# Kernel tuning notes

Hardware: AMD Instinct MI355X
Metric: run time of the kernel (lower is better)

The kernel has to match this reference:

```python
import jax, jax.numpy as jnp
import numpy as np

D_MODEL = 1024
N_HEADS = 16
D_K = D_MODEL // N_HEADS


def setup_inputs() -> dict:
    key = jax.random.key(0)
    ks = jax.random.split(key, 9)
    B, S = 2, 2048
    scale = 1.0 / np.sqrt(D_MODEL)
    inp = {
        "X": jax.random.normal(ks[0], (B, S, D_MODEL), dtype=jnp.float32),
        "Wq": jax.random.normal(ks[1], (D_MODEL, D_MODEL), dtype=jnp.float32) * scale,
        "bq": jnp.zeros((D_MODEL,), dtype=jnp.float32),
        "Wk": jax.random.normal(ks[2], (D_MODEL, D_MODEL), dtype=jnp.float32) * scale,
        "bk": jnp.zeros((D_MODEL,), dtype=jnp.float32),
        "Wv": jax.random.normal(ks[3], (D_MODEL, D_MODEL), dtype=jnp.float32) * scale,
        "bv": jnp.zeros((D_MODEL,), dtype=jnp.float32),
        "Wo": jax.random.normal(ks[4], (D_MODEL, D_MODEL), dtype=jnp.float32) * scale,
        "bo": jnp.zeros((D_MODEL,), dtype=jnp.float32),
    }
    return inp


def reference(X, Wq, bq, Wk, bk, Wv, bv, Wo, bo):
    B, S, _ = X.shape
    # QKV projections (torch Linear: x @ W.T + b; here W stored as [in, out])
    Q = X @ Wq + bq
    K = X @ Wk + bk
    V = X @ Wv + bv
    # [B, S, H, Dk] -> [B, H, S, Dk]
    def split_heads(t):
        return t.reshape(B, S, N_HEADS, D_K).transpose(0, 2, 1, 3)
    Q, K, V = split_heads(Q), split_heads(K), split_heads(V)
    scores = jnp.einsum('bhqd,bhkd->bhqk', Q, K) / jnp.sqrt(jnp.float32(D_K))
    attn = jax.nn.softmax(scores, axis=-1)
    out = jnp.einsum('bhqk,bhkd->bhqd', attn, V)  # [B, H, S, Dk]
    out = out.transpose(0, 2, 1, 3).reshape(B, S, D_MODEL)
    return out @ Wo + bo
```

## Files before the change

### kernel.cpp

```cpp
#include <hip/hip_runtime.h>
#include <hip/hip_bf16.h>


typedef __attribute__((ext_vector_type(8))) short short8;
typedef __attribute__((ext_vector_type(4))) float f32x4;
typedef unsigned short u16;
typedef unsigned int u32;

static __device__ __forceinline__ u16 f2bf(float f) {
    union { float f; u32 u; } c; c.f = f;
    u32 u = c.u;
    u32 r = u + 0x7fffu + ((u >> 16) & 1u);
    return (u16)(r >> 16);
}
static __device__ __forceinline__ float bf2f(u16 x) {
    union { u32 u; float f; } c; c.u = ((u32)x) << 16;
    return c.f;
}

#define GL1(p) ((const __attribute__((address_space(1))) void*)(p))
#define LD3(p) ((__attribute__((address_space(3))) void*)(p))
static __device__ __forceinline__ void gld16(const void* g, void* l) {
    __builtin_amdgcn_global_load_lds(GL1(g), LD3(l), 16, 0, 0);
}

#define Q_PRESCALE 0.18033688011112042f

__global__ __launch_bounds__(256) void convert_x(const float* __restrict__ X,
                                                 u16* __restrict__ Xb) {
    int i = (blockIdx.x * 256 + threadIdx.x) * 4;
    float4 v = *reinterpret_cast<const float4*>(X + i);
    ushort4 o;
    o.x = f2bf(v.x); o.y = f2bf(v.y); o.z = f2bf(v.z); o.w = f2bf(v.w);
    *reinterpret_cast<ushort4*>(Xb + i) = o;
}

__global__ __launch_bounds__(256) void transpose_w(
    const float* __restrict__ W0, const float* __restrict__ W1,
    const float* __restrict__ W2, const float* __restrict__ W3,
    u16* __restrict__ T0, u16* __restrict__ T1,
    u16* __restrict__ T2, u16* __restrict__ T3)
{
    const float* W; u16* T;
    switch (blockIdx.z) {
        case 0: W = W0; T = T0; break;
        case 1: W = W1; T = T1; break;
        case 2: W = W2; T = T2; break;
        default: W = W3; T = T3; break;
    }
    __shared__ float tile[64][65];
    int t = threadIdx.x;
    int k0 = blockIdx.y * 64, n0 = blockIdx.x * 64;
    int r = t / 16, c4 = (t % 16) * 4;
    #pragma unroll
    for (int p = 0; p < 4; p++) {
        int row = p * 16 + r;
        float4 v = *reinterpret_cast<const float4*>(W + (k0 + row) * 1024 + n0 + c4);
        tile[row][c4 + 0] = v.x; tile[row][c4 + 1] = v.y;
        tile[row][c4 + 2] = v.z; tile[row][c4 + 3] = v.w;
    }
    __syncthreads();
    #pragma unroll
    for (int p = 0; p < 4; p++) {
        int nrow = p * 16 + r;
        ushort4 o;
        o.x = f2bf(tile[c4 + 0][nrow]); o.y = f2bf(tile[c4 + 1][nrow]);
        o.z = f2bf(tile[c4 + 2][nrow]); o.w = f2bf(tile[c4 + 3][nrow]);
        *reinterpret_cast<ushort4*>(T + (n0 + nrow) * 1024 + k0 + c4) = o;
    }
}

__global__ __launch_bounds__(256) void gemm_qkv(
    const u16* __restrict__ Xb,
    const u16* __restrict__ Wtq, const u16* __restrict__ Wtk, const u16* __restrict__ Wtv,
    const float* __restrict__ bq, const float* __restrict__ bk, const float* __restrict__ bv,
    u16* __restrict__ Qb, u16* __restrict__ Kb, u16* __restrict__ Vb)
{
    const u16* Wt; const float* bias; u16* dst; float osc;
    if (blockIdx.z == 0)      { Wt = Wtq; bias = bq; dst = Qb; osc = Q_PRESCALE; }
    else if (blockIdx.z == 1) { Wt = Wtk; bias = bk; dst = Kb; osc = 1.0f; }
    else                      { Wt = Wtv; bias = bv; dst = Vb; osc = 1.0f; }

    __shared__ __align__(16) u16 As[128 * 32];
    __shared__ __align__(16) u16 Bs[128 * 32];
    int t = threadIdx.x;
    int w = t >> 6, lane = t & 63, l15 = lane & 15, quad = lane >> 4;
    int wm = (w >> 1) * 64, wn = (w & 1) * 64;
    int row0 = blockIdx.y * 128, col0 = blockIdx.x * 128;

    int drow = lane >> 2;
    int gc8 = ((lane & 3) ^ (drow & 3) ^ ((drow >> 2) & 3)) * 8;

    int asw = ((quad ^ (l15 & 3) ^ ((l15 >> 2) & 3)) & 3) * 8;

    f32x4 acc[4][4];
    #pragma unroll
    for (int i = 0; i < 4; i++)
        #pragma unroll
        for (int j = 0; j < 4; j++)
            acc[i][j] = (f32x4){0.f, 0.f, 0.f, 0.f};

    for (int k0 = 0; k0 < 1024; k0 += 32) {
        __syncthreads();
        #pragma unroll
        for (int q = 0; q < 2; q++) {
            int rr = w * 32 + q * 16;
            gld16(&Xb[(row0 + rr + drow) * 1024 + k0 + gc8], &As[rr * 32]);
            gld16(&Wt[(col0 + rr + drow) * 1024 + k0 + gc8], &Bs[rr * 32]);
        }
        __syncthreads();
        short8 a[4], b[4];
        #pragma unroll
        for (int i = 0; i < 4; i++)
            a[i] = *reinterpret_cast<const short8*>(&As[(wm + i * 16 + l15) * 32 + asw]);
        #pragma unroll
        for (int j = 0; j < 4; j++)
            b[j] = *reinterpret_cast<const short8*>(&Bs[(wn + j * 16 + l15) * 32 + asw]);
        #pragma unroll
        for (int i = 0; i < 4; i++)
            #pragma unroll
            for (int j = 0; j < 4; j++)
                acc[i][j] = __builtin_amdgcn_mfma_f32_16x16x32_bf16(a[i], b[j], acc[i][j], 0, 0, 0);
    }
    #pragma unroll
    for (int i = 0; i < 4; i++) {
        int rowb = row0 + wm + i * 16 + quad * 4;
        #pragma unroll
        for (int j = 0; j < 4; j++) {
            int col = col0 + wn + j * 16 + l15;
            float bb = bias[col];
            int h = col >> 6, d = col & 63;
            #pragma unroll
            for (int r = 0; r < 4; r++) {
                int gr = rowb + r;
                int b_ = gr >> 11, s = gr & 2047;
                dst[(((b_ << 4) + h) * 2048 + s) * 64 + d] = f2bf((acc[i][j][r] + bb) * osc);
            }
        }
    }
}

__global__ __launch_bounds__(256) void transpose_v(const u16* __restrict__ Vb,
                                                   u16* __restrict__ Vtg) {
    int bh = blockIdx.y;
    int s0 = blockIdx.x * 64;
    __shared__ u16 tile[64][72];
    int t = threadIdx.x;
    const u16* src = Vb + bh * (2048 * 64);
    u16* dst = Vtg + bh * (64 * 2048);
    int sl = t >> 3, d8 = (t & 7) * 8;
    #pragma unroll
    for (int p = 0; p < 2; p++) {
        int row = p * 32 + sl;
        *reinterpret_cast<uint4*>(&tile[row][d8]) =
            *reinterpret_cast<const uint4*>(&src[(s0 + row) * 64 + d8]);
    }
    __syncthreads();
    #pragma unroll
    for (int p = 0; p < 2; p++) {
        int dr = p * 32 + sl;
        union { u16 s[8]; uint4 v; } pk;
        #pragma unroll
        for (int i = 0; i < 8; i++) pk.s[i] = tile[d8 + i][dr];
        *reinterpret_cast<uint4*>(&dst[dr * 2048 + s0 + d8]) = pk.v;
    }
}

__global__ __launch_bounds__(256) void attn(
    const u16* __restrict__ Qb, const u16* __restrict__ Kb,
    const u16* __restrict__ Vtg, u16* __restrict__ Opart, float* __restrict__ Lsum)
{
    int qt = blockIdx.x, bh = blockIdx.y, sp = blockIdx.z;
    int b_ = bh >> 4, h = bh & 15;
    const u16* Qp = Qb + bh * (2048 * 64);
    const u16* Kp = Kb + bh * (2048 * 64);
    const u16* Vp = Vtg + bh * (64 * 2048);
    u16* Op = Opart + sp * (4096 * 1024);
    float* Lp = Lsum + sp * (32 * 2048) + bh * 2048;

    __shared__ __align__(16) u16 Ks[64 * 64];
    __shared__ __align__(16) u16 Vt[64 * 64];
    __shared__ __align__(16) u16 Ps[128 * 64];

    int t = threadIdx.x, w = t >> 6, lane = t & 63, l15 = lane & 15, quad = lane >> 4;

    short8 qf[2][2];
    #pragma unroll
    for (int f = 0; f < 2; f++)
        #pragma unroll
        for (int ds = 0; ds < 2; ds++)
            qf[f][ds] = *reinterpret_cast<const short8*>(
                &Qp[(qt * 128 + w * 32 + f * 16 + l15) * 64 + ds * 32 + quad * 8]);

    int di = lane >> 3;
    int dc8 = ((lane & 7) ^ di) * 8;

    int rl = l15 & 7, rh = l15 >> 3;
    int koff[4][2];
    #pragma unroll
    for (int j = 0; j < 4; j++)
        #pragma unroll
        for (int ds = 0; ds < 2; ds++)
            koff[j][ds] = (j * 2 + rh) * 512 + rl * 64 + (((ds * 4 + quad) ^ rl) & 7) * 8;

    int pwt[2][4];
    #pragma unroll
    for (int f = 0; f < 2; f++)
        #pragma unroll
        for (int j = 0; j < 4; j++)
            pwt[f][j] = (w * 32 + f * 16 + l15) * 64 +
                        (((2 * j + (quad >> 1)) ^ rl) * 8) + (quad & 1) * 4;
    int prt[2][2];
    #pragma unroll
    for (int f = 0; f < 2; f++)
        #pragma unroll
        for (int ks = 0; ks < 2; ks++)
            prt[f][ks] = (w * 32 + f * 16 + l15) * 64 + (((4 * ks + quad) ^ rl) * 8);

    f32x4 acc[2][4];
    float lsum[2] = {0.f, 0.f};
    #pragma unroll
    for (int f = 0; f < 2; f++)
        #pragma unroll
        for (int j = 0; j < 4; j++) acc[f][j] = (f32x4){0.f, 0.f, 0.f, 0.f};

    for (int kt = 0; kt < 16; kt++) {
        int kbase = sp * 1024 + kt * 64;
        __syncthreads();
        #pragma unroll
        for (int sg = 0; sg < 2; sg++) {
            int seg = w * 2 + sg;
            gld16(&Kp[(kbase + seg * 8 + di) * 64 + dc8], &Ks[seg * 512]);
            gld16(&Vp[(seg * 8 + di) * 2048 + kbase + dc8], &Vt[seg * 512]);
        }
        __syncthreads();

        f32x4 sc[2][4];
        #pragma unroll
        for (int j = 0; j < 4; j++) {
            f32x4 s0 = (f32x4){0.f, 0.f, 0.f, 0.f};
            f32x4 s1 = (f32x4){0.f, 0.f, 0.f, 0.f};
            #pragma unroll
            for (int ds = 0; ds < 2; ds++) {
                short8 kf = *reinterpret_cast<const short8*>(&Ks[koff[j][ds]]);
                s0 = __builtin_amdgcn_mfma_f32_16x16x32_bf16(kf, qf[0][ds], s0, 0, 0, 0);
                s1 = __builtin_amdgcn_mfma_f32_16x16x32_bf16(kf, qf[1][ds], s1, 0, 0, 0);
            }
            sc[0][j] = s0; sc[1][j] = s1;
        }

        #pragma unroll
        for (int f = 0; f < 2; f++)
            #pragma unroll
            for (int j = 0; j < 4; j++) {
                float p0 = __builtin_amdgcn_exp2f(sc[f][j][0]);
                float p1 = __builtin_amdgcn_exp2f(sc[f][j][1]);
                float p2 = __builtin_amdgcn_exp2f(sc[f][j][2]);
                float p3 = __builtin_amdgcn_exp2f(sc[f][j][3]);
                lsum[f] += (p0 + p1) + (p2 + p3);
                union { float fv; u32 uv; } c0, c1, c2, c3;
                c0.fv = p0; c1.fv = p1; c2.fv = p2; c3.fv = p3;
                uint2 pk;
                pk.x = ((c0.uv + 0x8000u) >> 16) | ((c1.uv + 0x8000u) & 0xffff0000u);
                pk.y = ((c2.uv + 0x8000u) >> 16) | ((c3.uv + 0x8000u) & 0xffff0000u);
                *reinterpret_cast<uint2*>(&Ps[pwt[f][j]]) = pk;
            }

        #pragma unroll
        for (int ks = 0; ks < 2; ks++) {
            short8 pf0 = *reinterpret_cast<const short8*>(&Ps[prt[0][ks]]);
            short8 pf1 = *reinterpret_cast<const short8*>(&Ps[prt[1][ks]]);
            #pragma unroll
            for (int j = 0; j < 4; j++) {
                short8 vf = *reinterpret_cast<const short8*>(&Vt[koff[j][ks]]);
                acc[0][j] = __builtin_amdgcn_mfma_f32_16x16x32_bf16(pf0, vf, acc[0][j], 0, 0, 0);
                acc[1][j] = __builtin_amdgcn_mfma_f32_16x16x32_bf16(pf1, vf, acc[1][j], 0, 0, 0);
            }
        }
    }

    #pragma unroll
    for (int f = 0; f < 2; f++) {
        float s = lsum[f];
        s += __shfl_xor(s, 16);
        s += __shfl_xor(s, 32);
        lsum[f] = s;
    }
    if (quad == 0) {
        #pragma unroll
        for (int f = 0; f < 2; f++)
            Lp[qt * 128 + w * 32 + f * 16 + l15] = lsum[f];
    }

    #pragma unroll
    for (int f = 0; f < 2; f++)
        #pragma unroll
        for (int j = 0; j < 4; j++)
            #pragma unroll
            for (int r = 0; r < 4; r++) {
                int srow = qt * 128 + w * 32 + f * 16 + quad * 4 + r;
                Op[(b_ * 2048 + srow) * 1024 + h * 64 + j * 16 + l15] = f2bf(acc[f][j][r]);
            }
}

__global__ __launch_bounds__(256) void combine(
    const u16* __restrict__ O0, const u16* __restrict__ O1,
    const float* __restrict__ L0, const float* __restrict__ L1,
    u16* __restrict__ Ob)
{
    int idx8 = (blockIdx.x * 256 + threadIdx.x) * 8;
    int row = idx8 >> 10, col = idx8 & 1023;
    int b_ = row >> 11, s = row & 2047, h = col >> 6;
    int li = (b_ * 16 + h) * 2048 + s;
    float inv = 1.0f / (L0[li] + L1[li]);
    union { uint4 v; u16 s[8]; } ua, ub, uo;
    ua.v = *reinterpret_cast<const uint4*>(&O0[idx8]);
    ub.v = *reinterpret_cast<const uint4*>(&O1[idx8]);
    #pragma unroll
    for (int i = 0; i < 8; i++)
        uo.s[i] = f2bf((bf2f(ua.s[i]) + bf2f(ub.s[i])) * inv);
    *reinterpret_cast<uint4*>(&Ob[idx8]) = uo.v;
}

__global__ __launch_bounds__(256) void gemm_out(
    const u16* __restrict__ Ob, const u16* __restrict__ Wto,
    const float* __restrict__ bo, float* __restrict__ out)
{
    __shared__ __align__(16) u16 As[128 * 32];
    __shared__ __align__(16) u16 Bs[128 * 32];
    int t = threadIdx.x;
    int w = t >> 6, lane = t & 63, l15 = lane & 15, quad = lane >> 4;
    int wm = (w >> 1) * 64, wn = (w & 1) * 64;
    int row0 = blockIdx.y * 128, col0 = blockIdx.x * 128;

    int drow = lane >> 2;
    int gc8 = ((lane & 3) ^ (drow & 3) ^ ((drow >> 2) & 3)) * 8;
    int asw = ((quad ^ (l15 & 3) ^ ((l15 >> 2) & 3)) & 3) * 8;

    f32x4 acc[4][4];
    #pragma unroll
    for (int i = 0; i < 4; i++)
        #pragma unroll
        for (int j = 0; j < 4; j++)
            acc[i][j] = (f32x4){0.f, 0.f, 0.f, 0.f};

    for (int k0 = 0; k0 < 1024; k0 += 32) {
        __syncthreads();
        #pragma unroll
        for (int q = 0; q < 2; q++) {
            int rr = w * 32 + q * 16;
            gld16(&Ob[(row0 + rr + drow) * 1024 + k0 + gc8], &As[rr * 32]);
            gld16(&Wto[(col0 + rr + drow) * 1024 + k0 + gc8], &Bs[rr * 32]);
        }
        __syncthreads();
        short8 a[4], b[4];
        #pragma unroll
        for (int i = 0; i < 4; i++)
            a[i] = *reinterpret_cast<const short8*>(&As[(wm + i * 16 + l15) * 32 + asw]);
        #pragma unroll
        for (int j = 0; j < 4; j++)
            b[j] = *reinterpret_cast<const short8*>(&Bs[(wn + j * 16 + l15) * 32 + asw]);
        #pragma unroll
        for (int i = 0; i < 4; i++)
            #pragma unroll
            for (int j = 0; j < 4; j++)
                acc[i][j] = __builtin_amdgcn_mfma_f32_16x16x32_bf16(a[i], b[j], acc[i][j], 0, 0, 0);
    }
    #pragma unroll
    for (int i = 0; i < 4; i++) {
        int rowb = row0 + wm + i * 16 + quad * 4;
        #pragma unroll
        for (int j = 0; j < 4; j++) {
            int col = col0 + wn + j * 16 + l15;
            float bb = bo[col];
            #pragma unroll
            for (int r = 0; r < 4; r++)
                out[(rowb + r) * 1024 + col] = acc[i][j][r] + bb;
        }
    }
}

extern "C" void kernel_launch(void* const* d_in, const int* in_sizes, int n_in,
                              void* d_out, int out_size, void* d_ws, size_t ws_size,
                              hipStream_t stream) {
    const float* X  = (const float*)d_in[0];
    const float* Wq = (const float*)d_in[1];
    const float* bq = (const float*)d_in[2];
    const float* Wk = (const float*)d_in[3];
    const float* bk = (const float*)d_in[4];
    const float* Wv = (const float*)d_in[5];
    const float* bv = (const float*)d_in[6];
    const float* Wo = (const float*)d_in[7];
    const float* bo = (const float*)d_in[8];
    float* out = (float*)d_out;

    char* ws = (char*)d_ws;
    u16* Xb   = (u16*)(ws);
    u16* Wtq  = (u16*)(ws + (8u  << 20));
    u16* Wtk  = (u16*)(ws + (10u << 20));
    u16* Wtv  = (u16*)(ws + (12u << 20));
    u16* Wto  = (u16*)(ws + (14u << 20));
    u16* Qb   = (u16*)(ws + (16u << 20));
    u16* Kb   = (u16*)(ws + (24u << 20));
    u16* Vb   = (u16*)(ws + (32u << 20));
    u16* Vtg  = (u16*)(ws + (40u << 20));
    u16* Op   = (u16*)(ws + (48u << 20));
    float* Ls = (float*)(ws + (64u << 20));
    u16* Ob   = (u16*)(ws + (65u << 20));

    convert_x  <<<4096, 256, 0, stream>>>(X, Xb);
    transpose_w<<<dim3(16, 16, 4), 256, 0, stream>>>(Wq, Wk, Wv, Wo, Wtq, Wtk, Wtv, Wto);
    gemm_qkv   <<<dim3(8, 32, 3), 256, 0, stream>>>(Xb, Wtq, Wtk, Wtv, bq, bk, bv, Qb, Kb, Vb);
    transpose_v<<<dim3(32, 32), 256, 0, stream>>>(Vb, Vtg);
    attn       <<<dim3(16, 32, 2), 256, 0, stream>>>(Qb, Kb, Vtg, Op, Ls);
    combine    <<<2048, 256, 0, stream>>>(Op, Op + (4096 * 1024), Ls, Ls + (32 * 2048), Ob);
    gemm_out   <<<dim3(8, 32), 256, 0, stream>>>(Ob, Wto, bo, out);
}
```

Measured before the change: 225.8 us.

## Fuse prep kernels and write V transposed directly from QKV GEMM epilogue

Merges the X conversion and weight transpose into one prep launch, and has the QKV GEMM write V already transposed ([bh][d][s]) so the separate transpose_v kernel goes away. Q and K are now stored in natural [B*S, 1024] row-major layout, and the attention kernel indexes heads through a 1024 stride. The point is to cut two kernel launches and one full pass over V. It also switches the P-to-bf16 packing from round-to-nearest to truncation, which is cheaper but slightly less accurate.

Result: slower. 234.2 us (+3.7%).

```diff
diff --git a/kernel.cpp b/kernel.cpp
--- a/kernel.cpp
+++ b/kernel.cpp
@@ -26,31 +26,33 @@
 
 #define Q_PRESCALE 0.18033688011112042f
 
-__global__ __launch_bounds__(256) void convert_x(const float* __restrict__ X,
-                                                 u16* __restrict__ Xb) {
-    int i = (blockIdx.x * 256 + threadIdx.x) * 4;
-    float4 v = *reinterpret_cast<const float4*>(X + i);
-    ushort4 o;
-    o.x = f2bf(v.x); o.y = f2bf(v.y); o.z = f2bf(v.z); o.w = f2bf(v.w);
-    *reinterpret_cast<ushort4*>(Xb + i) = o;
-}
-
-__global__ __launch_bounds__(256) void transpose_w(
+__global__ __launch_bounds__(256) void prep(
+    const float* __restrict__ X, u16* __restrict__ Xb,
     const float* __restrict__ W0, const float* __restrict__ W1,
     const float* __restrict__ W2, const float* __restrict__ W3,
     u16* __restrict__ T0, u16* __restrict__ T1,
     u16* __restrict__ T2, u16* __restrict__ T3)
 {
+    int id = blockIdx.x;
+    int t = threadIdx.x;
+    if (id >= 1024) {
+        int i = (id - 1024) * 1024 + t * 4;
+        float4 v = *reinterpret_cast<const float4*>(X + i);
+        ushort4 o;
+        o.x = f2bf(v.x); o.y = f2bf(v.y); o.z = f2bf(v.z); o.w = f2bf(v.w);
+        *reinterpret_cast<ushort4*>(Xb + i) = o;
+        return;
+    }
     const float* W; u16* T;
-    switch (blockIdx.z) {
+    switch (id >> 8) {
         case 0: W = W0; T = T0; break;
         case 1: W = W1; T = T1; break;
         case 2: W = W2; T = T2; break;
         default: W = W3; T = T3; break;
     }
+    int rem = id & 255;
+    int n0 = (rem & 15) * 64, k0 = (rem >> 4) * 64;
     __shared__ float tile[64][65];
-    int t = threadIdx.x;
-    int k0 = blockIdx.y * 64, n0 = blockIdx.x * 64;
     int r = t / 16, c4 = (t % 16) * 4;
     #pragma unroll
     for (int p = 0; p < 4; p++) {
@@ -74,12 +76,12 @@
     const u16* __restrict__ Xb,
     const u16* __restrict__ Wtq, const u16* __restrict__ Wtk, const u16* __restrict__ Wtv,
     const float* __restrict__ bq, const float* __restrict__ bk, const float* __restrict__ bv,
-    u16* __restrict__ Qb, u16* __restrict__ Kb, u16* __restrict__ Vb)
+    u16* __restrict__ Qn, u16* __restrict__ Kn, u16* __restrict__ Vtg)
 {
-    const u16* Wt; const float* bias; u16* dst; float osc;
-    if (blockIdx.z == 0)      { Wt = Wtq; bias = bq; dst = Qb; osc = Q_PRESCALE; }
-    else if (blockIdx.z == 1) { Wt = Wtk; bias = bk; dst = Kb; osc = 1.0f; }
-    else                      { Wt = Wtv; bias = bv; dst = Vb; osc = 1.0f; }
+    const u16* Wt; const float* bias;
+    if (blockIdx.z == 0)      { Wt = Wtq; bias = bq; }
+    else if (blockIdx.z == 1) { Wt = Wtk; bias = bk; }
+    else                      { Wt = Wtv; bias = bv; }
 
     __shared__ __align__(16) u16 As[128 * 32];
     __shared__ __align__(16) u16 Bs[128 * 32];
@@ -90,7 +92,6 @@
 
     int drow = lane >> 2;
     int gc8 = ((lane & 3) ^ (drow & 3) ^ ((drow >> 2) & 3)) * 8;
-
     int asw = ((quad ^ (l15 & 3) ^ ((l15 >> 2) & 3)) & 3) * 8;
 
     f32x4 acc[4][4];
@@ -122,58 +123,49 @@
             for (int j = 0; j < 4; j++)
                 acc[i][j] = __builtin_amdgcn_mfma_f32_16x16x32_bf16(a[i], b[j], acc[i][j], 0, 0, 0);
     }
-    #pragma unroll
-    for (int i = 0; i < 4; i++) {
-        int rowb = row0 + wm + i * 16 + quad * 4;
-        #pragma unroll
-        for (int j = 0; j < 4; j++) {
-            int col = col0 + wn + j * 16 + l15;
-            float bb = bias[col];
-            int h = col >> 6, d = col & 63;
-            #pragma unroll
-            for (int r = 0; r < 4; r++) {
-                int gr = rowb + r;
-                int b_ = gr >> 11, s = gr & 2047;
-                dst[(((b_ << 4) + h) * 2048 + s) * 64 + d] = f2bf((acc[i][j][r] + bb) * osc);
-            }
-        }
-    }
-}
-
-__global__ __launch_bounds__(256) void transpose_v(const u16* __restrict__ Vb,
-                                                   u16* __restrict__ Vtg) {
-    int bh = blockIdx.y;
-    int s0 = blockIdx.x * 64;
-    __shared__ u16 tile[64][72];
-    int t = threadIdx.x;
-    const u16* src = Vb + bh * (2048 * 64);
-    u16* dst = Vtg + bh * (64 * 2048);
-    int sl = t >> 3, d8 = (t & 7) * 8;
-    #pragma unroll
-    for (int p = 0; p < 2; p++) {
-        int row = p * 32 + sl;
-        *reinterpret_cast<uint4*>(&tile[row][d8]) =
-            *reinterpret_cast<const uint4*>(&src[(s0 + row) * 64 + d8]);
-    }
-    __syncthreads();
-    #pragma unroll
-    for (int p = 0; p < 2; p++) {
-        int dr = p * 32 + sl;
-        union { u16 s[8]; uint4 v; } pk;
-        #pragma unroll
-        for (int i = 0; i < 8; i++) pk.s[i] = tile[d8 + i][dr];
-        *reinterpret_cast<uint4*>(&dst[dr * 2048 + s0 + d8]) = pk.v;
+
+    if (blockIdx.z == 2) {
+        #pragma unroll
+        for (int i = 0; i < 4; i++) {
+            int gr = row0 + wm + i * 16 + quad * 4;
+            int b_ = gr >> 11, s = gr & 2047;
+            #pragma unroll
+            for (int j = 0; j < 4; j++) {
+                int col = col0 + wn + j * 16 + l15;
+                int h = col >> 6, d = col & 63;
+                float bb = bias[col];
+                ushort4 pk;
+                pk.x = f2bf(acc[i][j][0] + bb);
+                pk.y = f2bf(acc[i][j][1] + bb);
+                pk.z = f2bf(acc[i][j][2] + bb);
+                pk.w = f2bf(acc[i][j][3] + bb);
+                *reinterpret_cast<ushort4*>(&Vtg[((b_ * 16 + h) * 64 + d) * 2048 + s]) = pk;
+            }
+        }
+    } else {
+        u16* dst = (blockIdx.z == 0) ? Qn : Kn;
+        float osc = (blockIdx.z == 0) ? Q_PRESCALE : 1.0f;
+        #pragma unroll
+        for (int i = 0; i < 4; i++) {
+            int rowb = row0 + wm + i * 16 + quad * 4;
+            #pragma unroll
+            for (int j = 0; j < 4; j++) {
+                int col = col0 + wn + j * 16 + l15;
+                float bb = bias[col];
+                #pragma unroll
+                for (int r = 0; r < 4; r++)
+                    dst[(rowb + r) * 1024 + col] = f2bf((acc[i][j][r] + bb) * osc);
+            }
+        }
     }
 }
 
 __global__ __launch_bounds__(256) void attn(
-    const u16* __restrict__ Qb, const u16* __restrict__ Kb,
+    const u16* __restrict__ Qn, const u16* __restrict__ Kn,
     const u16* __restrict__ Vtg, u16* __restrict__ Opart, float* __restrict__ Lsum)
 {
     int qt = blockIdx.x, bh = blockIdx.y, sp = blockIdx.z;
     int b_ = bh >> 4, h = bh & 15;
-    const u16* Qp = Qb + bh * (2048 * 64);
-    const u16* Kp = Kb + bh * (2048 * 64);
     const u16* Vp = Vtg + bh * (64 * 2048);
     u16* Op = Opart + sp * (4096 * 1024);
     float* Lp = Lsum + sp * (32 * 2048) + bh * 2048;
@@ -190,7 +182,8 @@
         #pragma unroll
         for (int ds = 0; ds < 2; ds++)
             qf[f][ds] = *reinterpret_cast<const short8*>(
-                &Qp[(qt * 128 + w * 32 + f * 16 + l15) * 64 + ds * 32 + quad * 8]);
+                &Qn[(b_ * 2048 + qt * 128 + w * 32 + f * 16 + l15) * 1024 +
+                    h * 64 + ds * 32 + quad * 8]);
 
     int di = lane >> 3;
     int dc8 = ((lane & 7) ^ di) * 8;
@@ -230,7 +223,8 @@
         #pragma unroll
         for (int sg = 0; sg < 2; sg++) {
             int seg = w * 2 + sg;
-            gld16(&Kp[(kbase + seg * 8 + di) * 64 + dc8], &Ks[seg * 512]);
+            gld16(&Kn[(b_ * 2048 + kbase + seg * 8 + di) * 1024 + h * 64 + dc8],
+                  &Ks[seg * 512]);
             gld16(&Vp[(seg * 8 + di) * 2048 + kbase + dc8], &Vt[seg * 512]);
         }
         __syncthreads();
@@ -261,8 +255,8 @@
                 union { float fv; u32 uv; } c0, c1, c2, c3;
                 c0.fv = p0; c1.fv = p1; c2.fv = p2; c3.fv = p3;
                 uint2 pk;
-                pk.x = ((c0.uv + 0x8000u) >> 16) | ((c1.uv + 0x8000u) & 0xffff0000u);
-                pk.y = ((c2.uv + 0x8000u) >> 16) | ((c3.uv + 0x8000u) & 0xffff0000u);
+                pk.x = (c0.uv >> 16) | (c1.uv & 0xffff0000u);
+                pk.y = (c2.uv >> 16) | (c3.uv & 0xffff0000u);
                 *reinterpret_cast<uint2*>(&Ps[pwt[f][j]]) = pk;
             }
 
@@ -400,19 +394,16 @@
     u16* Wtk  = (u16*)(ws + (10u << 20));
     u16* Wtv  = (u16*)(ws + (12u << 20));
     u16* Wto  = (u16*)(ws + (14u << 20));
-    u16* Qb   = (u16*)(ws + (16u << 20));
-    u16* Kb   = (u16*)(ws + (24u << 20));
-    u16* Vb   = (u16*)(ws + (32u << 20));
-    u16* Vtg  = (u16*)(ws + (40u << 20));
-    u16* Op   = (u16*)(ws + (48u << 20));
-    float* Ls = (float*)(ws + (64u << 20));
-    u16* Ob   = (u16*)(ws + (65u << 20));
-
-    convert_x  <<<4096, 256, 0, stream>>>(X, Xb);
-    transpose_w<<<dim3(16, 16, 4), 256, 0, stream>>>(Wq, Wk, Wv, Wo, Wtq, Wtk, Wtv, Wto);
-    gemm_qkv   <<<dim3(8, 32, 3), 256, 0, stream>>>(Xb, Wtq, Wtk, Wtv, bq, bk, bv, Qb, Kb, Vb);
-    transpose_v<<<dim3(32, 32), 256, 0, stream>>>(Vb, Vtg);
-    attn       <<<dim3(16, 32, 2), 256, 0, stream>>>(Qb, Kb, Vtg, Op, Ls);
-    combine    <<<2048, 256, 0, stream>>>(Op, Op + (4096 * 1024), Ls, Ls + (32 * 2048), Ob);
-    gemm_out   <<<dim3(8, 32), 256, 0, stream>>>(Ob, Wto, bo, out);
-}
+    u16* Qn   = (u16*)(ws + (16u << 20));
+    u16* Kn   = (u16*)(ws + (24u << 20));
+    u16* Vtg  = (u16*)(ws + (32u << 20));
+    u16* Op   = (u16*)(ws + (40u << 20));
+    float* Ls = (float*)(ws + (56u << 20));
+    u16* Ob   = (u16*)(ws + (57u << 20));
+
+    prep     <<<5120, 256, 0, stream>>>(X, Xb, Wq, Wk, Wv, Wo, Wtq, Wtk, Wtv, Wto);
+    gemm_qkv <<<dim3(8, 32, 3), 256, 0, stream>>>(Xb, Wtq, Wtk, Wtv, bq, bk, bv, Qn, Kn, Vtg);
+    attn     <<<dim3(16, 32, 2), 256, 0, stream>>>(Qn, Kn, Vtg, Op, Ls);
+    combine  <<<2048, 256, 0, stream>>>(Op, Op + (4096 * 1024), Ls, Ls + (32 * 2048), Ob);
+    gemm_out <<<dim3(8, 32), 256, 0, stream>>>(Ob, Wto, bo, out);
+}
```
